# Performance work log

Hardware: AMD Instinct MI355X
Metric: run time of the kernel (lower is better)

The kernel has to match this reference:

```python
import jax, jax.numpy as jnp
import numpy as np
from functools import partial

B, C, H, W = 64, 3, 64, 64
D = 64            # hidden_dim == slot dim
S = 7             # num_slots
ITERS = 3
EPS_ATTN = 1e-8
MLP_HID = 128     # max(dim, 128)


def conv5_same(x, w, b):
    # x: [B, Cin, H, W], w: [Cout, Cin, 5, 5]
    y = jax.lax.conv_general_dilated(
        x, w, window_strides=(1, 1), padding='SAME',
        dimension_numbers=('NCHW', 'OIHW', 'NCHW'))
    return y + b[None, :, None, None]


def layernorm(x, w, b, eps):
    mu = jnp.mean(x, axis=-1, keepdims=True)
    var = jnp.var(x, axis=-1, keepdims=True)
    return (x - mu) * jax.lax.rsqrt(var + eps) * w + b


def build_grid(h, w):
    rr = jnp.linspace(0.0, 1.0, h)
    cc = jnp.linspace(0.0, 1.0, w)
    g = jnp.stack(jnp.meshgrid(rr, cc, indexing='ij'), axis=-1)  # [H,W,2]
    return jnp.concatenate([g, 1.0 - g], axis=-1)                # [H,W,4]


def setup_inputs() -> dict:
    key = jax.random.key(0)
    ks = jax.random.split(key, 32)
    sc = lambda fan: 1.0 / np.sqrt(fan)
    inp = {
        'image': jax.random.normal(ks[0], (B, C, H, W), jnp.float32),
        'slots_noise': jax.random.normal(ks[1], (B, S, D), jnp.float32),
        'conv0_w': jax.random.normal(ks[2], (D, 3, 5, 5), jnp.float32) * sc(3 * 25),
        'conv0_b': jnp.zeros((D,), jnp.float32),
        'conv1_w': jax.random.normal(ks[3], (D, D, 5, 5), jnp.float32) * sc(D * 25),
        'conv1_b': jnp.zeros((D,), jnp.float32),
        'conv2_w': jax.random.normal(ks[4], (D, D, 5, 5), jnp.float32) * sc(D * 25),
        'conv2_b': jnp.zeros((D,), jnp.float32),
        'conv3_w': jax.random.normal(ks[5], (D, D, 5, 5), jnp.float32) * sc(D * 25),
        'conv3_b': jnp.zeros((D,), jnp.float32),
        'pos_w': jax.random.normal(ks[6], (D, 4), jnp.float32) * sc(4),
        'pos_b': jnp.zeros((D,), jnp.float32),
        'fc1_w': jax.random.normal(ks[7], (D, D), jnp.float32) * sc(D),
        'fc1_b': jnp.zeros((D,), jnp.float32),
        'fc2_w': jax.random.normal(ks[8], (D, D), jnp.float32) * sc(D),
        'fc2_b': jnp.zeros((D,), jnp.float32),
        'slots_mu': jax.random.uniform(ks[9], (1, 1, D), jnp.float32, -0.3, 0.3),
        'slots_log_sigma': jax.random.uniform(ks[10], (1, 1, D), jnp.float32, -0.3, 0.3),
        'q_w': jax.random.normal(ks[11], (D, D), jnp.float32) * sc(D),
        'k_w': jax.random.normal(ks[12], (D, D), jnp.float32) * sc(D),
        'v_w': jax.random.normal(ks[13], (D, D), jnp.float32) * sc(D),
        'gru_w_ih': jax.random.normal(ks[14], (3 * D, D), jnp.float32) * sc(D),
        'gru_w_hh': jax.random.normal(ks[15], (3 * D, D), jnp.float32) * sc(D),
        'gru_b_ih': jnp.zeros((3 * D,), jnp.float32),
        'gru_b_hh': jnp.zeros((3 * D,), jnp.float32),
        'mlp1_w': jax.random.normal(ks[16], (MLP_HID, D), jnp.float32) * sc(D),
        'mlp1_b': jnp.zeros((MLP_HID,), jnp.float32),
        'mlp2_w': jax.random.normal(ks[17], (D, MLP_HID), jnp.float32) * sc(MLP_HID),
        'mlp2_b': jnp.zeros((D,), jnp.float32),
        'ln_in_w': jnp.ones((D,), jnp.float32),
        'ln_in_b': jnp.zeros((D,), jnp.float32),
        'ln_slots_w': jnp.ones((D,), jnp.float32),
        'ln_slots_b': jnp.zeros((D,), jnp.float32),
        'ln_ff_w': jnp.ones((D,), jnp.float32),
        'ln_ff_b': jnp.zeros((D,), jnp.float32),
    }
    return inp


def reference(image, slots_noise, conv0_w, conv0_b, conv1_w, conv1_b,
              conv2_w, conv2_b, conv3_w, conv3_b, pos_w, pos_b,
              fc1_w, fc1_b, fc2_w, fc2_b, slots_mu, slots_log_sigma,
              q_w, k_w, v_w, gru_w_ih, gru_w_hh, gru_b_ih, gru_b_hh,
              mlp1_w, mlp1_b, mlp2_w, mlp2_b,
              ln_in_w, ln_in_b, ln_slots_w, ln_slots_b, ln_ff_w, ln_ff_b):
    b = image.shape[0]
    # --- CNN encoder ---
    x = jax.nn.relu(conv5_same(image, conv0_w, conv0_b))
    x = jax.nn.relu(conv5_same(x, conv1_w, conv1_b))
    x = jax.nn.relu(conv5_same(x, conv2_w, conv2_b))
    x = jax.nn.relu(conv5_same(x, conv3_w, conv3_b))
    x = jnp.transpose(x, (0, 2, 3, 1))                 # [B,H,W,D]
    pos = build_grid(x.shape[1], x.shape[2]) @ pos_w.T + pos_b
    x = x + pos[None]
    x = x.reshape(b, -1, D)                            # [B,N,D]
    # LayerNorm over (N, D) jointly, fresh affine (w=1, b=0), eps=1e-5
    mu = jnp.mean(x, axis=(1, 2), keepdims=True)
    var = jnp.var(x, axis=(1, 2), keepdims=True)
    x = (x - mu) * jax.lax.rsqrt(var + 1e-5)
    # --- fc MLP ---
    x = jax.nn.relu(x @ fc1_w.T + fc1_b) @ fc2_w.T + fc2_b
    # --- Slot attention ---
    scale = D ** (-0.5)
    slots = slots_mu + jnp.exp(slots_log_sigma) * slots_noise  # [B,S,D]
    inp = layernorm(x, ln_in_w, ln_in_b, 1e-3)
    k = inp @ k_w.T                                    # [B,N,D]
    v = inp @ v_w.T
    for _ in range(ITERS):
        slots_prev = slots
        q = layernorm(slots, ln_slots_w, ln_slots_b, 1e-3) @ q_w.T  # [B,S,D]
        dots = jnp.einsum('bid,bjd->bij', q, k) * scale             # [B,S,N]
        attn = jax.nn.softmax(dots, axis=1) + EPS_ATTN              # over slots
        attn = attn / jnp.sum(attn, axis=-1, keepdims=True)
        updates = jnp.einsum('bjd,bij->bid', v, attn)               # [B,S,D]
        # GRUCell(updates, slots_prev)
        gi = updates @ gru_w_ih.T + gru_b_ih                        # [B,S,3D]
        gh = slots_prev @ gru_w_hh.T + gru_b_hh
        i_r, i_z, i_n = jnp.split(gi, 3, axis=-1)
        h_r, h_z, h_n = jnp.split(gh, 3, axis=-1)
        r = jax.nn.sigmoid(i_r + h_r)
        z = jax.nn.sigmoid(i_z + h_z)
        n = jnp.tanh(i_n + r * h_n)
        slots = (1.0 - z) * n + z * slots_prev
        # residual MLP
        h = layernorm(slots, ln_ff_w, ln_ff_b, 1e-3)
        slots = slots + (jax.nn.relu(h @ mlp1_w.T + mlp1_b) @ mlp2_w.T + mlp2_b)
    return slots
```

## Files before the change

### kernel.cpp

```cpp
#include <hip/hip_runtime.h>

#define HW 64
#define BATCH 64
#define DDIM 64
#define NSLOT 7
#define NPOS 4096

typedef __attribute__((ext_vector_type(8))) short short8;
typedef __attribute__((ext_vector_type(4))) short short4v;
typedef __attribute__((ext_vector_type(4))) float floatx4;

__device__ __forceinline__ float wave_sum(float x) {
  #pragma unroll
  for (int o = 32; o >= 1; o >>= 1) x += __shfl_xor(x, o, 64);
  return x;
}

__device__ __forceinline__ unsigned short f2bf(float f) {
  unsigned int u = __float_as_uint(f);
  return (unsigned short)((u + 0x7fffu + ((u >> 16) & 1u)) >> 16);
}
__device__ __forceinline__ float bf2f(unsigned short u) {
  return __uint_as_float(((unsigned int)u) << 16);
}
__device__ __forceinline__ short4v pack4(float a, float b, float c, float d) {
  short4v s;
  s.x = (short)f2bf(a); s.y = (short)f2bf(b);
  s.z = (short)f2bf(c); s.w = (short)f2bf(d);
  return s;
}

__global__ __launch_bounds__(256) void prep_w(
    const float* __restrict__ w1, const float* __restrict__ w2,
    const float* __restrict__ w3, unsigned short* __restrict__ wp)
{
  int idx = blockIdx.x * 256 + threadIdx.x;
  if (idx >= 3 * 102400) return;
  int L = idx / 102400;
  int rem = idx - L * 102400;
  int tap = rem >> 12;
  int r2  = rem & 4095;
  int ks = r2 >> 11;
  int mt = (r2 >> 9) & 3;
  int l  = (r2 >> 3) & 63;
  int j  = r2 & 7;
  int oc  = mt * 16 + (l & 15);
  int cin = (ks * 4 + (l >> 4)) * 8 + j;
  const float* w = (L == 0) ? w1 : (L == 1) ? w2 : w3;
  wp[idx] = f2bf(w[(oc * 64 + cin) * 25 + tap]);
}

__global__ __launch_bounds__(256) void prep_fcw(
    const float* __restrict__ f1, const float* __restrict__ f2,
    const float* __restrict__ kw, const float* __restrict__ vw,
    unsigned short* __restrict__ dst)
{
  int idx = blockIdx.x * 256 + threadIdx.x;
  int mat = idx >> 12;
  int r = idx & 4095;
  int ks = r >> 11;
  int mt = (r >> 9) & 3;
  int l  = (r >> 3) & 63;
  int j  = r & 7;
  int oc = mt * 16 + (l & 15);
  int in = (ks * 4 + (l >> 4)) * 8 + j;
  const float* src = (mat == 0) ? f1 : (mat == 1) ? f2 : (mat == 2) ? kw : vw;
  dst[idx] = f2bf(src[oc * 64 + in]);
}

__global__ void prep_s1(const float* __restrict__ f1, float* __restrict__ s1)
{
  int oc = threadIdx.x;
  float s = 0.f;
  for (int k = 0; k < 64; k++) s += f1[oc * 64 + k];
  s1[oc] = s;
}

__global__ __launch_bounds__(256) void conv0_relu(
    const float* __restrict__ in, const float* __restrict__ wgt,
    const float* __restrict__ bias, unsigned short* __restrict__ out)
{
  constexpr int TH = 8, TW = 32, OCT = 16, CIN = 3;
  __shared__ __align__(16) float sIn[CIN][TH + 4][40];
  __shared__ __align__(16) float sW[CIN][25][OCT];

  const int bx = blockIdx.x;
  const int tx = bx & 1;
  const int ty = (bx >> 1) & 7;
  const int b  = bx >> 4;
  const int ocb = blockIdx.y * OCT;
  const int x0 = tx * TW, y0 = ty * TH;
  const int tid = threadIdx.x;

  const int sq  = tid & 63;
  const int ocq = tid >> 6;
  const int yy  = sq >> 3;
  const int xx4 = (sq & 7) << 2;
  const int oc0 = ocq << 2;

  float acc[4][4];
  #pragma unroll
  for (int o = 0; o < 4; o++)
    #pragma unroll
    for (int x = 0; x < 4; x++) acc[o][x] = 0.f;

  for (int idx = tid; idx < CIN * 12 * 36; idx += 256) {
    int c  = idx % 36;
    int r  = (idx / 36) % 12;
    int ci = idx / (36 * 12);
    int gy = y0 - 2 + r, gx = x0 - 2 + c;
    float v = 0.f;
    if (gy >= 0 && gy < HW && gx >= 0 && gx < HW)
      v = in[((b * CIN + ci) * HW + gy) * HW + gx];
    sIn[ci][r][c] = v;
  }
  for (int idx = tid; idx < CIN * 25 * OCT; idx += 256) {
    int oc  = idx & 15;
    int tap = (idx >> 4) % 25;
    int ci  = idx / (16 * 25);
    sW[ci][tap][oc] = wgt[((ocb + oc) * CIN + ci) * 25 + tap];
  }
  __syncthreads();

  for (int ci = 0; ci < CIN; ci++) {
    #pragma unroll
    for (int dy = 0; dy < 5; dy++) {
      const float* rp = &sIn[ci][yy + dy][xx4];
      float4 a0 = *(const float4*)rp;
      float4 a1 = *(const float4*)(rp + 4);
      float vals[8] = {a0.x, a0.y, a0.z, a0.w, a1.x, a1.y, a1.z, a1.w};
      #pragma unroll
      for (int dx = 0; dx < 5; dx++) {
        float4 wv = *(const float4*)&sW[ci][dy * 5 + dx][oc0];
        float wa[4] = {wv.x, wv.y, wv.z, wv.w};
        #pragma unroll
        for (int o = 0; o < 4; o++)
          #pragma unroll
          for (int x = 0; x < 4; x++)
            acc[o][x] += wa[o] * vals[dx + x];
      }
    }
  }

  float bb[4];
  #pragma unroll
  for (int o = 0; o < 4; o++) bb[o] = bias[ocb + oc0 + o];
  #pragma unroll
  for (int x = 0; x < 4; x++) {
    int pos = (b << 12) + (y0 + yy) * 64 + (x0 + xx4 + x);
    *(short4v*)&out[pos * 64 + ocb + oc0] =
        pack4(fmaxf(acc[0][x] + bb[0], 0.f), fmaxf(acc[1][x] + bb[1], 0.f),
              fmaxf(acc[2][x] + bb[2], 0.f), fmaxf(acc[3][x] + bb[3], 0.f));
  }
}

template<int FUSE_POS>
__global__ __launch_bounds__(256) void conv_mfma(
    const unsigned short* __restrict__ in, const unsigned short* __restrict__ wp,
    const float* __restrict__ bias, unsigned short* __restrict__ out,
    const float* __restrict__ pos_w, const float* __restrict__ pos_b,
    float* __restrict__ stats)
{
  extern __shared__ short lds[];
  short* sIn = lds;
  uint4* sWu0 = (uint4*)(lds + 25600);
  uint4* sWu1 = sWu0 + 512;

  const int tid = threadIdx.x;
  const int b   = blockIdx.x >> 4;
  const int tile = blockIdx.x & 15;
  const int y0 = (tile >> 2) * 16, x0 = (tile & 3) * 16;

  const uint4* in4 = (const uint4*)in;
  for (int idx = tid; idx < 3200; idx += 256) {
    int p = idx >> 3, c = idx & 7;
    int py = p / 20, px = p - py * 20;
    int gy = y0 - 2 + py, gx = x0 - 2 + px;
    uint4 v = {0u, 0u, 0u, 0u};
    if ((unsigned)gy < 64u && (unsigned)gx < 64u)
      v = in4[(((b << 12) + (gy << 6) + gx) << 3) + c];
    *(uint4*)&sIn[(p << 6) + ((c ^ (p & 7)) << 3)] = v;
  }
  const uint4* wg = (const uint4*)wp;
  sWu0[tid] = wg[tid];
  sWu0[256 + tid] = wg[256 + tid];
  uint4 r0 = wg[512 + tid];
  uint4 r1 = wg[512 + 256 + tid];
  __syncthreads();

  const int w  = tid >> 6;
  const int l  = tid & 63;
  const int lx = l & 15;
  const int kq = l >> 4;
  const int w4 = w * 4;

  floatx4 zero4 = {0.f, 0.f, 0.f, 0.f};
  floatx4 acc[4][4];
  #pragma unroll
  for (int yy = 0; yy < 4; yy++)
    #pragma unroll
    for (int mt = 0; mt < 4; mt++) acc[yy][mt] = zero4;

  int dy = 0, dx = 0;
  #pragma unroll 1
  for (int t = 0; t < 25; ++t) {
    uint4* cur = (t & 1) ? sWu1 : sWu0;
    if (t < 24) {
      uint4* alt = (t & 1) ? sWu0 : sWu1;
      alt[tid] = r0;
      alt[256 + tid] = r1;
    }
    if (t < 23) {
      r0 = wg[(t + 2) * 512 + tid];
      r1 = wg[(t + 2) * 512 + 256 + tid];
    }
    const int ix = lx + dx;
    #pragma unroll
    for (int ks = 0; ks < 2; ++ks) {
      const int kc = ks * 4 + kq;
      short8 Bf[4];
      #pragma unroll
      for (int yy = 0; yy < 4; ++yy) {
        int p = (w4 + yy + dy) * 20 + ix;
        Bf[yy] = *(const short8*)&sIn[(p << 6) + ((kc ^ (p & 7)) << 3)];
      }
      #pragma unroll
      for (int mt = 0; mt < 4; ++mt) {
        uint4 Af4 = cur[(ks * 4 + mt) * 64 + l];
        #pragma unroll
        for (int yy = 0; yy < 4; ++yy)
          acc[yy][mt] = __builtin_amdgcn_mfma_f32_16x16x32_bf16(
              *(const short8*)&Af4, Bf[yy], acc[yy][mt], 0, 0, 0);
      }
    }
    if (t < 24) __syncthreads();
    if (++dx == 5) { dx = 0; ++dy; }
  }

  float4 bv[4];
  #pragma unroll
  for (int mt = 0; mt < 4; ++mt) bv[mt] = *(const float4*)&bias[mt * 16 + kq * 4];

  float4 pw[4][4];  float pb[4][4];
  if (FUSE_POS) {
    #pragma unroll
    for (int mt = 0; mt < 4; ++mt)
      #pragma unroll
      for (int r = 0; r < 4; ++r) {
        int d = mt * 16 + kq * 4 + r;
        pw[mt][r] = *(const float4*)&pos_w[d * 4];
        pb[mt][r] = pos_b[d];
      }
  }

  const int x = x0 + lx;
  const float cx = x * (1.0f / 63.0f);
  float lsum = 0.f, lsq = 0.f;

  #pragma unroll
  for (int yy = 0; yy < 4; ++yy) {
    const int y = y0 + w4 + yy;
    const float ry = y * (1.0f / 63.0f);
    const int base = ((b << 12) + y * 64 + x) * 64;
    #pragma unroll
    for (int mt = 0; mt < 4; ++mt) {
      float v[4];
      #pragma unroll
      for (int r = 0; r < 4; ++r) {
        float f = fmaxf(acc[yy][mt][r] + bv[mt][r], 0.f);
        if (FUSE_POS) {
          f += ry * pw[mt][r].x + cx * pw[mt][r].y + (1.f - ry) * pw[mt][r].z +
               (1.f - cx) * pw[mt][r].w + pb[mt][r];
          lsum += f; lsq += f * f;
        }
        v[r] = f;
      }
      *(short4v*)&out[base + mt * 16 + kq * 4] = pack4(v[0], v[1], v[2], v[3]);
    }
  }

  if (FUSE_POS) {
    lsum = wave_sum(lsum);
    lsq  = wave_sum(lsq);
    if (l == 0) {
      atomicAdd(&stats[b * 2], lsum);
      atomicAdd(&stats[b * 2 + 1], lsq);
    }
  }
}

__global__ void finalize_stats(const float* __restrict__ stats, float* __restrict__ ms)
{
  int b = threadIdx.x;
  float s = stats[b * 2], q = stats[b * 2 + 1];
  float mean = s * (1.0f / 262144.f);
  float var  = q * (1.0f / 262144.f) - mean * mean;
  ms[b * 2] = mean;
  ms[b * 2 + 1] = rsqrtf(var + 1e-5f);
}

__global__ __launch_bounds__(256) void fc_mfma(
    const unsigned short* __restrict__ xb, const float* __restrict__ ms,
    const unsigned short* __restrict__ wall, const float* __restrict__ fc1_b,
    const float* __restrict__ s1, const float* __restrict__ fc2_b,
    const float* __restrict__ ln_w, const float* __restrict__ ln_b,
    unsigned short* __restrict__ kb, unsigned short* __restrict__ vb)
{
  __shared__ short sA[64 * 64];
  __shared__ uint4 sW[2048];
  const int tid = threadIdx.x;
  const int w = tid >> 6, l = tid & 63, lx = l & 15, kq = l >> 4;
  const int p0 = blockIdx.x * 64;
  const int b  = blockIdx.x >> 6;
  const int w16 = w * 16;
  const float mean = ms[b * 2], rstd = ms[b * 2 + 1];
  const float rmu = rstd * mean;

  const uint4* wg = (const uint4*)wall;
  #pragma unroll
  for (int i = 0; i < 8; ++i) sW[i * 256 + tid] = wg[i * 256 + tid];

  {
    const uint4* x4 = (const uint4*)xb;
    int r0 = w16 + (l >> 3), c = l & 7;
    uint4 v0 = x4[((p0 + r0) << 3) + c];
    uint4 v1 = x4[((p0 + r0 + 8) << 3) + c];
    *(uint4*)&sA[(r0 << 6) + ((c ^ (r0 & 7)) << 3)] = v0;
    int r1 = r0 + 8;
    *(uint4*)&sA[(r1 << 6) + ((c ^ (r1 & 7)) << 3)] = v1;
  }
  __syncthreads();

  const int brow = w16 + lx;
  floatx4 zero4 = {0.f, 0.f, 0.f, 0.f};

  #define GEMM64(MATI, ACC)                                                   \
    {                                                                         \
      _Pragma("unroll")                                                       \
      for (int ks = 0; ks < 2; ++ks) {                                        \
        int ch = (ks * 4 + kq) ^ (brow & 7);                                  \
        short8 Bf = *(const short8*)&sA[(brow << 6) + (ch << 3)];             \
        _Pragma("unroll")                                                     \
        for (int mt = 0; mt < 4; ++mt) {                                      \
          uint4 Af = sW[(MATI) * 512 + (ks * 4 + mt) * 64 + l];               \
          ACC[mt] = __builtin_amdgcn_mfma_f32_16x16x32_bf16(                  \
              *(const short8*)&Af, Bf, ACC[mt], 0, 0, 0);                     \
        }                                                                     \
      }                                                                       \
    }

  #define LDSW(MT, SV)                                                        \
    {                                                                         \
      int ch = ((MT) * 2 + (kq >> 1)) ^ (brow & 7);                           \
      *(short4v*)&sA[(brow << 6) + (ch << 3) + ((kq & 1) << 2)] = (SV);       \
    }

  floatx4 a1[4] = {zero4, zero4, zero4, zero4};
  GEMM64(0, a1);
  #pragma unroll
  for (int mt = 0; mt < 4; ++mt) {
    float4 b1v = *(const float4*)&fc1_b[mt * 16 + kq * 4];
    float4 s1v = *(const float4*)&s1[mt * 16 + kq * 4];
    float v[4];
    v[0] = fmaxf(rstd * a1[mt][0] - rmu * s1v.x + b1v.x, 0.f);
    v[1] = fmaxf(rstd * a1[mt][1] - rmu * s1v.y + b1v.y, 0.f);
    v[2] = fmaxf(rstd * a1[mt][2] - rmu * s1v.z + b1v.z, 0.f);
    v[3] = fmaxf(rstd * a1[mt][3] - rmu * s1v.w + b1v.w, 0.f);
    LDSW(mt, pack4(v[0], v[1], v[2], v[3]));
  }

  floatx4 a2[4] = {zero4, zero4, zero4, zero4};
  GEMM64(1, a2);
  float y2[4][4];
  float ps = 0.f, pq = 0.f;
  #pragma unroll
  for (int mt = 0; mt < 4; ++mt) {
    float4 b2v = *(const float4*)&fc2_b[mt * 16 + kq * 4];
    float bb[4] = {b2v.x, b2v.y, b2v.z, b2v.w};
    #pragma unroll
    for (int r = 0; r < 4; ++r) {
      float y = a2[mt][r] + bb[r];
      y2[mt][r] = y;
      ps += y; pq += y * y;
    }
  }
  ps += __shfl_xor(ps, 16, 64);  ps += __shfl_xor(ps, 32, 64);
  pq += __shfl_xor(pq, 16, 64);  pq += __shfl_xor(pq, 32, 64);
  float mu2 = ps * (1.f / 64.f);
  float rs2 = rsqrtf(pq * (1.f / 64.f) - mu2 * mu2 + 1e-3f);
  #pragma unroll
  for (int mt = 0; mt < 4; ++mt) {
    float4 lwv = *(const float4*)&ln_w[mt * 16 + kq * 4];
    float4 lbv = *(const float4*)&ln_b[mt * 16 + kq * 4];
    float v[4];
    v[0] = (y2[mt][0] - mu2) * rs2 * lwv.x + lbv.x;
    v[1] = (y2[mt][1] - mu2) * rs2 * lwv.y + lbv.y;
    v[2] = (y2[mt][2] - mu2) * rs2 * lwv.z + lbv.z;
    v[3] = (y2[mt][3] - mu2) * rs2 * lwv.w + lbv.w;
    LDSW(mt, pack4(v[0], v[1], v[2], v[3]));
  }

  floatx4 a3[4] = {zero4, zero4, zero4, zero4};
  GEMM64(2, a3);
  const int gbase = ((p0 + brow) << 6) + kq * 4;
  #pragma unroll
  for (int mt = 0; mt < 4; ++mt)
    *(short4v*)&kb[gbase + mt * 16] = pack4(a3[mt][0], a3[mt][1], a3[mt][2], a3[mt][3]);

  floatx4 a4[4] = {zero4, zero4, zero4, zero4};
  GEMM64(3, a4);
  #pragma unroll
  for (int mt = 0; mt < 4; ++mt)
    *(short4v*)&vb[gbase + mt * 16] = pack4(a4[mt][0], a4[mt][1], a4[mt][2], a4[mt][3]);

  #undef GEMM64
  #undef LDSW
}

__global__ __launch_bounds__(256) void slots_init(
    const float* __restrict__ mu, const float* __restrict__ ls,
    const float* __restrict__ noise, float* __restrict__ slots)
{
  int idx = blockIdx.x * 256 + threadIdx.x;
  if (idx < BATCH * NSLOT * DDIM) {
    int d = idx & 63;
    slots[idx] = mu[d] + expf(ls[d]) * noise[idx];
  }
}

__global__ __launch_bounds__(64) void compute_q(
    const float* __restrict__ slots, const float* __restrict__ lnw,
    const float* __restrict__ lnb, const float* __restrict__ q_w,
    float* __restrict__ qout, float* __restrict__ U, float* __restrict__ T)
{
  __shared__ float sLn[64];
  const int bs = blockIdx.x;
  const int l = threadIdx.x;
  U[bs * 64 + l] = 0.f;
  if (l == 0) T[bs] = 0.f;
  float v = slots[bs * 64 + l];
  float m = wave_sum(v) * (1.f / 64.f);
  float dv = v - m;
  float var = wave_sum(dv * dv) * (1.f / 64.f);
  sLn[l] = dv * rsqrtf(var + 1e-3f) * lnw[l] + lnb[l];
  __syncthreads();
  float acc = 0.f;
  #pragma unroll
  for (int e = 0; e < 64; e += 4) {
    float4 w4 = *(const float4*)&q_w[l * 64 + e];
    acc += w4.x * sLn[e] + w4.y * sLn[e + 1] + w4.z * sLn[e + 2] + w4.w * sLn[e + 3];
  }
  qout[bs * 64 + l] = acc;
}

__global__ __launch_bounds__(256) void attn_dots_mfma(
    const unsigned short* __restrict__ kb, const float* __restrict__ q,
    float* __restrict__ P, float* __restrict__ T)
{
  __shared__ short sQ[16 * 64];
  const int b  = blockIdx.x >> 4;
  const int jt = blockIdx.x & 15;
  const int tid = threadIdx.x;
  const int w = tid >> 6, l = tid & 63, lx = l & 15, kq = l >> 4;
  floatx4 zero4 = {0.f, 0.f, 0.f, 0.f};

  for (int i = tid; i < 1024; i += 256) {
    int s = i >> 6, d = i & 63;
    sQ[i] = (s < 7) ? (short)f2bf(q[(b * 7 + s) * 64 + d]) : (short)0;
  }
  __syncthreads();

  uint4 qA[2];
  #pragma unroll
  for (int ks = 0; ks < 2; ++ks)
    qA[ks] = *(const uint4*)&sQ[lx * 64 + (ks * 4 + kq) * 8];

  const uint4* kb4 = (const uint4*)kb;
  const int row0 = kq * 4;
  const int j0 = jt * 256 + w * 64;
  float tacc[4] = {0.f, 0.f, 0.f, 0.f};

  #pragma unroll
  for (int jh = 0; jh < 4; ++jh) {
    const int j = j0 + jh * 16 + lx;
    floatx4 d4 = zero4;
    #pragma unroll
    for (int ks = 0; ks < 2; ++ks) {
      uint4 kB = kb4[(((b << 12) + j) << 3) + ks * 4 + kq];
      d4 = __builtin_amdgcn_mfma_f32_16x16x32_bf16(
          *(const short8*)&qA[ks], *(const short8*)&kB, d4, 0, 0, 0);
    }
    float e[4];
    float mx = -1e30f;
    #pragma unroll
    for (int r = 0; r < 4; ++r) {
      e[r] = (row0 + r < 7) ? d4[r] * 0.125f : -1e30f;
      mx = fmaxf(mx, e[r]);
    }
    mx = fmaxf(mx, __shfl_xor(mx, 16, 64));
    mx = fmaxf(mx, __shfl_xor(mx, 32, 64));
    float sum = 0.f;
    #pragma unroll
    for (int r = 0; r < 4; ++r) {
      e[r] = (row0 + r < 7) ? __expf(e[r] - mx) : 0.f;
      sum += e[r];
    }
    sum += __shfl_xor(sum, 16, 64);
    sum += __shfl_xor(sum, 32, 64);
    float inv = 1.f / sum;
    #pragma unroll
    for (int r = 0; r < 4; ++r) {
      if (row0 + r < 7) {
        float p = e[r] * inv + 1e-8f;
        tacc[r] += p;
        P[(b * 7 + row0 + r) * NPOS + j] = p;
      }
    }
  }

  #pragma unroll
  for (int r = 0; r < 4; ++r) {
    if (row0 + r < 7) {
      float t = tacc[r];
      t += __shfl_xor(t, 1, 64);  t += __shfl_xor(t, 2, 64);
      t += __shfl_xor(t, 4, 64);  t += __shfl_xor(t, 8, 64);
      if (lx == 0) atomicAdd(&T[b * 7 + row0 + r], t);
    }
  }
}

__global__ __launch_bounds__(448) void attn_updates(
    const float* __restrict__ P, const unsigned short* __restrict__ vb,
    float* __restrict__ U)
{
  const int b = blockIdx.x >> 3;
  const int chunk = blockIdx.x & 7;
  const int s = threadIdx.x / 64;
  const int l = threadIdx.x & 63;
  const int j0 = chunk * 512;
  const float* Pr = &P[(b * NSLOT + s) * NPOS + j0];
  const unsigned short* vr = &vb[(b * NPOS + j0) * 64 + l];
  float acc = 0.f;
  for (int j = 0; j < 512; j++) acc += Pr[j] * bf2f(vr[j * 64]);
  atomicAdd(&U[(b * NSLOT + s) * 64 + l], acc);
}

__global__ __launch_bounds__(192) void gru_mlp(
    const float* __restrict__ U, const float* __restrict__ T,
    const float* __restrict__ w_ih, const float* __restrict__ w_hh,
    const float* __restrict__ b_ih, const float* __restrict__ b_hh,
    const float* __restrict__ lnfw, const float* __restrict__ lnfb,
    const float* __restrict__ m1w, const float* __restrict__ m1b,
    const float* __restrict__ m2w, const float* __restrict__ m2b,
    float* __restrict__ slots)
{
  __shared__ float sU[64], sSp[64], sGi[192], sGh[192], sH[64], sLn[64], sHid[128];
  const int bs = blockIdx.x;
  const int t = threadIdx.x;

  if (t < 64) {
    sU[t] = U[bs * 64 + t] / T[bs];
    sSp[t] = slots[bs * 64 + t];
  }
  __syncthreads();
  {
    float gi = b_ih[t], gh = b_hh[t];
    #pragma unroll
    for (int d = 0; d < 64; d += 4) {
      float4 wi = *(const float4*)&w_ih[t * 64 + d];
      float4 wh = *(const float4*)&w_hh[t * 64 + d];
      gi += wi.x * sU[d] + wi.y * sU[d + 1] + wi.z * sU[d + 2] + wi.w * sU[d + 3];
      gh += wh.x * sSp[d] + wh.y * sSp[d + 1] + wh.z * sSp[d + 2] + wh.w * sSp[d + 3];
    }
    sGi[t] = gi; sGh[t] = gh;
  }
  __syncthreads();
  if (t < 64) {
    float r = 1.f / (1.f + expf(-(sGi[t] + sGh[t])));
    float z = 1.f / (1.f + expf(-(sGi[64 + t] + sGh[64 + t])));
    float n = tanhf(sGi[128 + t] + r * sGh[128 + t]);
    float h = (1.f - z) * n + z * sSp[t];
    sH[t] = h;
    float m = wave_sum(h) * (1.f / 64.f);
    float dv = h - m;
    float var = wave_sum(dv * dv) * (1.f / 64.f);
    sLn[t] = dv * rsqrtf(var + 1e-3f) * lnfw[t] + lnfb[t];
  }
  __syncthreads();
  if (t < 128) {
    float a = m1b[t];
    #pragma unroll
    for (int d = 0; d < 64; d += 4) {
      float4 w = *(const float4*)&m1w[t * 64 + d];
      a += w.x * sLn[d] + w.y * sLn[d + 1] + w.z * sLn[d + 2] + w.w * sLn[d + 3];
    }
    sHid[t] = fmaxf(a, 0.f);
  }
  __syncthreads();
  if (t < 64) {
    float a = m2b[t];
    #pragma unroll
    for (int k = 0; k < 128; k += 4) {
      float4 w = *(const float4*)&m2w[t * 128 + k];
      a += w.x * sHid[k] + w.y * sHid[k + 1] + w.z * sHid[k + 2] + w.w * sHid[k + 3];
    }
    slots[bs * 64 + t] = sH[t] + a;
  }
}

extern "C" void kernel_launch(void* const* d_in, const int* in_sizes, int n_in,
                              void* d_out, int out_size, void* d_ws, size_t ws_size,
                              hipStream_t stream)
{
  const float* image    = (const float*)d_in[0];
  const float* noise    = (const float*)d_in[1];
  const float* conv0_w  = (const float*)d_in[2];
  const float* conv0_b  = (const float*)d_in[3];
  const float* conv1_w  = (const float*)d_in[4];
  const float* conv1_b  = (const float*)d_in[5];
  const float* conv2_w  = (const float*)d_in[6];
  const float* conv2_b  = (const float*)d_in[7];
  const float* conv3_w  = (const float*)d_in[8];
  const float* conv3_b  = (const float*)d_in[9];
  const float* pos_w    = (const float*)d_in[10];
  const float* pos_b    = (const float*)d_in[11];
  const float* fc1_w    = (const float*)d_in[12];
  const float* fc1_b    = (const float*)d_in[13];
  const float* fc2_w    = (const float*)d_in[14];
  const float* fc2_b    = (const float*)d_in[15];
  const float* slots_mu = (const float*)d_in[16];
  const float* slots_ls = (const float*)d_in[17];
  const float* q_w      = (const float*)d_in[18];
  const float* k_w      = (const float*)d_in[19];
  const float* v_w      = (const float*)d_in[20];
  const float* gru_w_ih = (const float*)d_in[21];
  const float* gru_w_hh = (const float*)d_in[22];
  const float* gru_b_ih = (const float*)d_in[23];
  const float* gru_b_hh = (const float*)d_in[24];
  const float* mlp1_w   = (const float*)d_in[25];
  const float* mlp1_b   = (const float*)d_in[26];
  const float* mlp2_w   = (const float*)d_in[27];
  const float* mlp2_b   = (const float*)d_in[28];
  const float* ln_in_w  = (const float*)d_in[29];
  const float* ln_in_b  = (const float*)d_in[30];
  const float* ln_sl_w  = (const float*)d_in[31];
  const float* ln_sl_b  = (const float*)d_in[32];
  const float* ln_ff_w  = (const float*)d_in[33];
  const float* ln_ff_b  = (const float*)d_in[34];

  float* ws = (float*)d_ws;
  float* R1   = ws;
  float* R2   = R1 + 16777216;
  float* Pbuf = R2 + 16777216;
  float* qbuf  = Pbuf + 1835008;
  float* slots = qbuf + 28672;
  float* Ubuf  = slots + 28672;
  float* Tbuf  = Ubuf + 28672;
  float* stats = Tbuf + 448;
  float* ms    = stats + 128;

  unsigned short* Wp  = (unsigned short*)Pbuf;
  unsigned short* wfc = Wp + 307200;
  float* s1f = (float*)(wfc + 16384);
  unsigned short* Y0 = (unsigned short*)R1;
  unsigned short* Y1 = (unsigned short*)R2;
  unsigned short* xb = (unsigned short*)R2;
  unsigned short* kb = (unsigned short*)R1;
  unsigned short* vb = kb + 16777216;

  prep_w<<<1200, 256, 0, stream>>>(conv1_w, conv2_w, conv3_w, Wp);
  prep_fcw<<<64, 256, 0, stream>>>(fc1_w, fc2_w, k_w, v_w, wfc);
  prep_s1<<<1, 64, 0, stream>>>(fc1_w, s1f);
  hipMemsetAsync(stats, 0, 128 * sizeof(float), stream);

  dim3 cgrid(1024, 4);
  conv0_relu<<<cgrid, 256, 0, stream>>>(image, conv0_w, conv0_b, Y0);
  conv_mfma<0><<<1024, 256, 67584, stream>>>(Y0, Wp,          conv1_b, Y1,
                                             nullptr, nullptr, nullptr);
  conv_mfma<0><<<1024, 256, 67584, stream>>>(Y1, Wp + 102400, conv2_b, Y0,
                                             nullptr, nullptr, nullptr);
  conv_mfma<1><<<1024, 256, 67584, stream>>>(Y0, Wp + 204800, conv3_b, xb,
                                             pos_w, pos_b, stats);
  finalize_stats<<<1, 64, 0, stream>>>(stats, ms);

  fc_mfma<<<4096, 256, 0, stream>>>(xb, ms, wfc, fc1_b, s1f, fc2_b,
                                    ln_in_w, ln_in_b, kb, vb);

  slots_init<<<112, 256, 0, stream>>>(slots_mu, slots_ls, noise, slots);

  for (int it = 0; it < 3; it++) {
    compute_q<<<448, 64, 0, stream>>>(slots, ln_sl_w, ln_sl_b, q_w, qbuf,
                                      Ubuf, Tbuf);
    attn_dots_mfma<<<1024, 256, 0, stream>>>(kb, qbuf, Pbuf, Tbuf);
    attn_updates<<<512, 448, 0, stream>>>(Pbuf, vb, Ubuf);
    gru_mlp<<<448, 192, 0, stream>>>(Ubuf, Tbuf, gru_w_ih, gru_w_hh, gru_b_ih,
                                     gru_b_hh, ln_ff_w, ln_ff_b, mlp1_w, mlp1_b,
                                     mlp2_w, mlp2_b, slots);
  }

  hipMemcpyAsync(d_out, slots, 28672 * sizeof(float), hipMemcpyDeviceToDevice, stream);
}
```

Before: 600.2 us.

## Split conv input channels into two chunks to halve LDS footprint

The MFMA conv kernel now processes the 64 input channels in two 32-channel passes, staging only half of the input tile and half of each tap's weights in shared memory. The input tile uses a padded 40-short row stride instead of the XOR swizzle. This cuts the LDS allocation from about 66KB to about 39KB so more blocks can reside per CU. The cost is reloading the halo tile twice and doubling the number of loop iterations and barriers.

```diff
diff --git a/kernel.cpp b/kernel.cpp
--- a/kernel.cpp
+++ b/kernel.cpp
@@ -163,30 +163,13 @@
 {
   extern __shared__ short lds[];
   short* sIn = lds;
-  uint4* sWu0 = (uint4*)(lds + 25600);
-  uint4* sWu1 = sWu0 + 512;
+  uint4* sWu0 = (uint4*)(lds + 16000);
+  uint4* sWu1 = sWu0 + 256;
 
   const int tid = threadIdx.x;
   const int b   = blockIdx.x >> 4;
   const int tile = blockIdx.x & 15;
   const int y0 = (tile >> 2) * 16, x0 = (tile & 3) * 16;
-
-  const uint4* in4 = (const uint4*)in;
-  for (int idx = tid; idx < 3200; idx += 256) {
-    int p = idx >> 3, c = idx & 7;
-    int py = p / 20, px = p - py * 20;
-    int gy = y0 - 2 + py, gx = x0 - 2 + px;
-    uint4 v = {0u, 0u, 0u, 0u};
-    if ((unsigned)gy < 64u && (unsigned)gx < 64u)
-      v = in4[(((b << 12) + (gy << 6) + gx) << 3) + c];
-    *(uint4*)&sIn[(p << 6) + ((c ^ (p & 7)) << 3)] = v;
-  }
-  const uint4* wg = (const uint4*)wp;
-  sWu0[tid] = wg[tid];
-  sWu0[256 + tid] = wg[256 + tid];
-  uint4 r0 = wg[512 + tid];
-  uint4 r1 = wg[512 + 256 + tid];
-  __syncthreads();
 
   const int w  = tid >> 6;
   const int l  = tid & 63;
@@ -201,40 +184,54 @@
     #pragma unroll
     for (int mt = 0; mt < 4; mt++) acc[yy][mt] = zero4;
 
-  int dy = 0, dx = 0;
+  const uint4* in4 = (const uint4*)in;
+  const uint4* wg = (const uint4*)wp;
+
   #pragma unroll 1
-  for (int t = 0; t < 25; ++t) {
-    uint4* cur = (t & 1) ? sWu1 : sWu0;
-    if (t < 24) {
-      uint4* alt = (t & 1) ? sWu0 : sWu1;
-      alt[tid] = r0;
-      alt[256 + tid] = r1;
-    }
-    if (t < 23) {
-      r0 = wg[(t + 2) * 512 + tid];
-      r1 = wg[(t + 2) * 512 + 256 + tid];
-    }
-    const int ix = lx + dx;
-    #pragma unroll
-    for (int ks = 0; ks < 2; ++ks) {
-      const int kc = ks * 4 + kq;
+  for (int chunk = 0; chunk < 2; ++chunk) {
+    __syncthreads();
+    for (int idx = tid; idx < 1600; idx += 256) {
+      int p = idx >> 2, u = idx & 3;
+      int py = p / 20, px = p - py * 20;
+      int gy = y0 - 2 + py, gx = x0 - 2 + px;
+      uint4 v = {0u, 0u, 0u, 0u};
+      if ((unsigned)gy < 64u && (unsigned)gx < 64u)
+        v = in4[(((b << 12) + (gy << 6) + gx) << 3) + chunk * 4 + u];
+      *(uint4*)&sIn[p * 40 + u * 8] = v;
+    }
+    const int base = chunk * 256;
+    sWu0[tid] = wg[base + tid];
+    uint4 r0 = wg[base + 512 + tid];
+    __syncthreads();
+
+    int dy = 0, dx = 0;
+    #pragma unroll 1
+    for (int t = 0; t < 25; ++t) {
+      uint4* cur = (t & 1) ? sWu1 : sWu0;
+      if (t < 24) {
+        uint4* alt = (t & 1) ? sWu0 : sWu1;
+        alt[tid] = r0;
+      }
+      if (t < 23)
+        r0 = wg[base + (t + 2) * 512 + tid];
+      const int ix = lx + dx;
       short8 Bf[4];
       #pragma unroll
       for (int yy = 0; yy < 4; ++yy) {
         int p = (w4 + yy + dy) * 20 + ix;
-        Bf[yy] = *(const short8*)&sIn[(p << 6) + ((kc ^ (p & 7)) << 3)];
+        Bf[yy] = *(const short8*)&sIn[p * 40 + kq * 8];
       }
       #pragma unroll
       for (int mt = 0; mt < 4; ++mt) {
-        uint4 Af4 = cur[(ks * 4 + mt) * 64 + l];
+        uint4 Af4 = cur[mt * 64 + l];
         #pragma unroll
         for (int yy = 0; yy < 4; ++yy)
           acc[yy][mt] = __builtin_amdgcn_mfma_f32_16x16x32_bf16(
               *(const short8*)&Af4, Bf[yy], acc[yy][mt], 0, 0, 0);
       }
-    }
-    if (t < 24) __syncthreads();
-    if (++dx == 5) { dx = 0; ++dy; }
+      if (t < 24) __syncthreads();
+      if (++dx == 5) { dx = 0; ++dy; }
+    }
   }
 
   float4 bv[4];
@@ -675,11 +672,11 @@
 
   dim3 cgrid(1024, 4);
   conv0_relu<<<cgrid, 256, 0, stream>>>(image, conv0_w, conv0_b, Y0);
-  conv_mfma<0><<<1024, 256, 67584, stream>>>(Y0, Wp,          conv1_b, Y1,
+  conv_mfma<0><<<1024, 256, 40192, stream>>>(Y0, Wp,          conv1_b, Y1,
                                              nullptr, nullptr, nullptr);
-  conv_mfma<0><<<1024, 256, 67584, stream>>>(Y1, Wp + 102400, conv2_b, Y0,
+  conv_mfma<0><<<1024, 256, 40192, stream>>>(Y1, Wp + 102400, conv2_b, Y0,
                                              nullptr, nullptr, nullptr);
-  conv_mfma<1><<<1024, 256, 67584, stream>>>(Y0, Wp + 204800, conv3_b, xb,
+  conv_mfma<1><<<1024, 256, 40192, stream>>>(Y0, Wp + 204800, conv3_b, xb,
                                              pos_w, pos_b, stats);
   finalize_stats<<<1, 64, 0, stream>>>(stats, ms);
 
```

Result: slower. 634.6 us (+5.7%).

## Fuse attention softmax and update matmul, store V transposed for MFMA

Applied to the files above, without the earlier changes.

Merges the dots/softmax kernel and the updates kernel into one. The bf16 attention probabilities stay in shared memory and feed a second MFMA against a transposed V layout, which the fc kernel now writes directly. This removes the fp32 P buffer round trip through global memory and the scalar, strided updates loop. In exchange, the fc kernel's V stores become scattered 2-byte writes, probabilities are rounded to bf16, and there are more atomics per block.

```diff
diff --git a/kernel.cpp b/kernel.cpp
--- a/kernel.cpp
+++ b/kernel.cpp
@@ -304,7 +304,7 @@
     const unsigned short* __restrict__ wall, const float* __restrict__ fc1_b,
     const float* __restrict__ s1, const float* __restrict__ fc2_b,
     const float* __restrict__ ln_w, const float* __restrict__ ln_b,
-    unsigned short* __restrict__ kb, unsigned short* __restrict__ vb)
+    unsigned short* __restrict__ kb, unsigned short* __restrict__ vT)
 {
   __shared__ short sA[64 * 64];
   __shared__ uint4 sW[2048];
@@ -312,6 +312,7 @@
   const int w = tid >> 6, l = tid & 63, lx = l & 15, kq = l >> 4;
   const int p0 = blockIdx.x * 64;
   const int b  = blockIdx.x >> 6;
+  const int posb = (blockIdx.x & 63) * 64;
   const int w16 = w * 16;
   const float mean = ms[b * 2], rstd = ms[b * 2 + 1];
   const float rmu = rstd * mean;
@@ -411,7 +412,9 @@
   GEMM64(3, a4);
   #pragma unroll
   for (int mt = 0; mt < 4; ++mt)
-    *(short4v*)&vb[gbase + mt * 16] = pack4(a4[mt][0], a4[mt][1], a4[mt][2], a4[mt][3]);
+    #pragma unroll
+    for (int r = 0; r < 4; ++r)
+      vT[((b << 6) + mt * 16 + kq * 4 + r) * 4096 + posb + brow] = f2bf(a4[mt][r]);
 
   #undef GEMM64
   #undef LDSW
@@ -453,11 +456,14 @@
   qout[bs * 64 + l] = acc;
 }
 
-__global__ __launch_bounds__(256) void attn_dots_mfma(
+__global__ __launch_bounds__(256) void attn_fused(
     const unsigned short* __restrict__ kb, const float* __restrict__ q,
-    float* __restrict__ P, float* __restrict__ T)
+    const unsigned short* __restrict__ vT,
+    float* __restrict__ U, float* __restrict__ T)
 {
   __shared__ short sQ[16 * 64];
+  __shared__ short sP[4][16 * 72];
+  __shared__ float sUr[4][7 * 64];
   const int b  = blockIdx.x >> 4;
   const int jt = blockIdx.x & 15;
   const int tid = threadIdx.x;
@@ -479,6 +485,7 @@
   const int row0 = kq * 4;
   const int j0 = jt * 256 + w * 64;
   float tacc[4] = {0.f, 0.f, 0.f, 0.f};
+  short* sPw = sP[w];
 
   #pragma unroll
   for (int jh = 0; jh < 4; ++jh) {
@@ -510,11 +517,9 @@
     float inv = 1.f / sum;
     #pragma unroll
     for (int r = 0; r < 4; ++r) {
-      if (row0 + r < 7) {
-        float p = e[r] * inv + 1e-8f;
-        tacc[r] += p;
-        P[(b * 7 + row0 + r) * NPOS + j] = p;
-      }
+      float p = (row0 + r < 7) ? e[r] * inv + 1e-8f : 0.f;
+      tacc[r] += p;
+      sPw[(row0 + r) * 72 + jh * 16 + lx] = (short)f2bf(p);
     }
   }
 
@@ -527,22 +532,33 @@
       if (lx == 0) atomicAdd(&T[b * 7 + row0 + r], t);
     }
   }
-}
-
-__global__ __launch_bounds__(448) void attn_updates(
-    const float* __restrict__ P, const unsigned short* __restrict__ vb,
-    float* __restrict__ U)
-{
-  const int b = blockIdx.x >> 3;
-  const int chunk = blockIdx.x & 7;
-  const int s = threadIdx.x / 64;
-  const int l = threadIdx.x & 63;
-  const int j0 = chunk * 512;
-  const float* Pr = &P[(b * NSLOT + s) * NPOS + j0];
-  const unsigned short* vr = &vb[(b * NPOS + j0) * 64 + l];
-  float acc = 0.f;
-  for (int j = 0; j < 512; j++) acc += Pr[j] * bf2f(vr[j * 64]);
-  atomicAdd(&U[(b * NSLOT + s) * 64 + l], acc);
+  __syncthreads();
+
+  floatx4 uacc[4] = {zero4, zero4, zero4, zero4};
+  #pragma unroll
+  for (int nt = 0; nt < 4; ++nt) {
+    #pragma unroll
+    for (int ks = 0; ks < 2; ++ks) {
+      short8 pa = *(const short8*)&sPw[lx * 72 + ks * 32 + kq * 8];
+      uint4 vB = *(const uint4*)&vT[((b << 6) + nt * 16 + lx) * 4096 +
+                                    j0 + ks * 32 + kq * 8];
+      uacc[nt] = __builtin_amdgcn_mfma_f32_16x16x32_bf16(
+          pa, *(const short8*)&vB, uacc[nt], 0, 0, 0);
+    }
+  }
+
+  #pragma unroll
+  for (int nt = 0; nt < 4; ++nt)
+    #pragma unroll
+    for (int r = 0; r < 4; ++r)
+      if (row0 + r < 7)
+        sUr[w][(row0 + r) * 64 + nt * 16 + lx] = uacc[nt][r];
+  __syncthreads();
+
+  for (int i = tid; i < 448; i += 256) {
+    float u = sUr[0][i] + sUr[1][i] + sUr[2][i] + sUr[3][i];
+    atomicAdd(&U[b * 448 + i], u);
+  }
 }
 
 __global__ __launch_bounds__(192) void gru_mlp(
@@ -666,7 +682,7 @@
   unsigned short* Y1 = (unsigned short*)R2;
   unsigned short* xb = (unsigned short*)R2;
   unsigned short* kb = (unsigned short*)R1;
-  unsigned short* vb = kb + 16777216;
+  unsigned short* vT = kb + 16777216;
 
   prep_w<<<1200, 256, 0, stream>>>(conv1_w, conv2_w, conv3_w, Wp);
   prep_fcw<<<64, 256, 0, stream>>>(fc1_w, fc2_w, k_w, v_w, wfc);
@@ -684,15 +700,14 @@
   finalize_stats<<<1, 64, 0, stream>>>(stats, ms);
 
   fc_mfma<<<4096, 256, 0, stream>>>(xb, ms, wfc, fc1_b, s1f, fc2_b,
-                                    ln_in_w, ln_in_b, kb, vb);
+                                    ln_in_w, ln_in_b, kb, vT);
 
   slots_init<<<112, 256, 0, stream>>>(slots_mu, slots_ls, noise, slots);
 
   for (int it = 0; it < 3; it++) {
     compute_q<<<448, 64, 0, stream>>>(slots, ln_sl_w, ln_sl_b, q_w, qbuf,
                                       Ubuf, Tbuf);
-    attn_dots_mfma<<<1024, 256, 0, stream>>>(kb, qbuf, Pbuf, Tbuf);
-    attn_updates<<<512, 448, 0, stream>>>(Pbuf, vb, Ubuf);
+    attn_fused<<<1024, 256, 0, stream>>>(kb, qbuf, vT, Ubuf, Tbuf);
     gru_mlp<<<448, 192, 0, stream>>>(Ubuf, Tbuf, gru_w_ih, gru_w_hh, gru_b_ih,
                                      gru_b_hh, ln_ff_w, ln_ff_b, mlp1_w, mlp1_b,
                                      mlp2_w, mlp2_b, slots);
```

Result: faster. 555.9 us (-7.4%).
